# Performance work log

Hardware: AMD Instinct MI355X
Metric: run time of the kernel (lower is better)

## Reference

```python
import jax, jax.numpy as jnp
import numpy as np

EPS = 1e-12  # F.normalize default eps


def _wn_weight(v, g):
    # torch weight_norm(dim=0) on Conv1d weight [out, in, 1]: w = g * v / ||v||_rows
    norm = jnp.sqrt(jnp.sum(v * v, axis=1, keepdims=True))
    return v * (g[:, None] / norm)


def _l2norm(x):
    n = jnp.sqrt(jnp.sum(x * x, axis=-1, keepdims=True))
    return x / jnp.maximum(n, EPS)


def setup_inputs() -> dict:
    key = jax.random.key(0)
    ks = jax.random.split(key, 4)
    B, D, T = 16, 1024, 4096
    CD, CS = 8, 1024
    return {
        "z": jax.random.normal(ks[0], (B, D, T), dtype=jnp.float32),
        "in_proj_v": jax.random.normal(ks[1], (CD, D), dtype=jnp.float32) * 0.02,
        "in_proj_g": jnp.ones((CD,), dtype=jnp.float32),
        "in_proj_b": jnp.zeros((CD,), dtype=jnp.float32),
        "out_proj_v": jax.random.normal(ks[2], (D, CD), dtype=jnp.float32) * 0.02,
        "out_proj_g": jnp.ones((D,), dtype=jnp.float32),
        "out_proj_b": jnp.zeros((D,), dtype=jnp.float32),
        "codebook": jax.random.normal(ks[3], (CS, CD), dtype=jnp.float32),
    }


def reference(z, in_proj_v, in_proj_g, in_proj_b, out_proj_v, out_proj_g, out_proj_b, codebook):
    B, D, T = z.shape
    CD = codebook.shape[1]

    # in_proj: 1x1 weight-normed conv == per-timestep linear
    w_in = _wn_weight(in_proj_v, in_proj_g)            # [CD, D]
    z_e = jnp.einsum('od,bdt->bot', w_in, z) + in_proj_b[None, :, None]  # [B, CD, T]

    # decode_latents: cosine-distance nearest neighbor in normalized space
    enc = jnp.transpose(z_e, (0, 2, 1)).reshape(B * T, CD)  # (b t) d
    enc_n = _l2norm(enc)
    cb_n = _l2norm(codebook)
    # dist = |e|^2 - 2 e.c + |c|^2 over normalized vectors
    dist = (jnp.sum(enc_n * enc_n, axis=1, keepdims=True)
            - 2.0 * enc_n @ cb_n.T
            + jnp.sum(cb_n * cb_n, axis=1)[None, :])       # [B*T, CS]
    indices = jnp.argmax(-dist, axis=1).reshape(B, T)      # [B, T]
    z_q = jnp.transpose(codebook[indices], (0, 2, 1))      # [B, CD, T] (un-normalized codebook gather)

    # losses (reduce over dims [1,2] -> per-batch)
    sg = jax.lax.stop_gradient
    commitment_loss = jnp.mean((z_e - sg(z_q)) ** 2, axis=(1, 2))
    codebook_loss = jnp.mean((z_q - sg(z_e)) ** 2, axis=(1, 2))

    # straight-through
    z_q_st = z_e + sg(z_q - z_e)

    w_out = _wn_weight(out_proj_v, out_proj_g)          # [D, CD]
    out = jnp.einsum('dc,bct->bdt', w_out, z_q_st) + out_proj_b[None, :, None]
    return out, commitment_loss, codebook_loss, indices, z_e
```

## Files before the change

kernel.cpp:

```cpp
#include <hip/hip_runtime.h>
#include <math.h>

#define BB 16
#define DD 1024
#define TT 4096
#define CD 8
#define CS 1024

#define OFF_LOSS_C 67108864
#define OFF_LOSS_B 67108880
#define OFF_IDX    67108896
#define OFF_ZE     67174432

#define WS_WIN  0
#define WS_WOUT 8192
#define WS_CBN  16384
#define WS_CS   24576

#define TILE_T 64

typedef float vfloat4 __attribute__((ext_vector_type(4)));

__global__ __launch_bounds__(256) void prep_kernel(
    const float* __restrict__ in_v,
    const float* __restrict__ in_g,
    const float* __restrict__ out_v,
    const float* __restrict__ out_g,
    const float* __restrict__ cb,
    float* __restrict__ ws)
{
    int bid = blockIdx.x, tid = threadIdx.x;
    if (bid < 8) {
        __shared__ float red[256];
        __shared__ float ssc;
        int o = bid;
        float p = 0.f;
        for (int k = tid; k < DD; k += 256) { float v = in_v[o*DD + k]; p += v*v; }
        red[tid] = p; __syncthreads();
        for (int s = 128; s > 0; s >>= 1) { if (tid < s) red[tid] += red[tid+s]; __syncthreads(); }
        if (tid == 0) ssc = in_g[o] / sqrtf(red[0]);
        __syncthreads();
        float scale = ssc;
        for (int d = tid; d < DD; d += 256)
            ws[WS_WIN + d*CD + o] = in_v[o*DD + d] * scale;
    } else if (bid < 12) {
        int d = (bid - 8) * 256 + tid;
        float v[CD]; float ssq = 0.f;
        #pragma unroll
        for (int c = 0; c < CD; ++c) { v[c] = out_v[d*CD + c]; ssq += v[c]*v[c]; }
        float s = out_g[d] / sqrtf(ssq);
        #pragma unroll
        for (int c = 0; c < CD; ++c) ws[WS_WOUT + d*CD + c] = v[c]*s;
    } else {
        int c = (bid - 12) * 256 + tid;
        double* csh = (double*)(ws + WS_CS);
        float v[CD]; float ssq = 0.f;
        #pragma unroll
        for (int j = 0; j < CD; ++j) { v[j] = cb[c*CD + j]; ssq += v[j]*v[j]; }
        float n = fmaxf(sqrtf(ssq), 1e-12f);
        double sq = 0.0;
        #pragma unroll
        for (int j = 0; j < CD; ++j) {
            float e = v[j] / n;
            ws[WS_CBN + c*CD + j] = e;
            sq = fma((double)e, (double)e, sq);
        }
        csh[c] = 0.5 * sq;
    }
}

__global__ __launch_bounds__(256, 4) void fused_kernel(
    const float* __restrict__ z,
    const float* __restrict__ in_b,
    const float* __restrict__ cb,
    const float* __restrict__ out_b,
    const float* __restrict__ ws,
    float* __restrict__ outb)
{
    __shared__ float  zpart[4][CD][TILE_T];
    __shared__ float  ze_s[CD][TILE_T];
    __shared__ float  nrm_s[TILE_T];
    __shared__ double best_s[4][TILE_T];
    __shared__ int    bidx_s[4][TILE_T];
    __shared__ __align__(16) float zq_s[CD][TILE_T];

    int tid  = threadIdx.x;
    int b    = blockIdx.y;
    int t0   = blockIdx.x * TILE_T;
    int tl   = tid & 63;
    int wv   = __builtin_amdgcn_readfirstlane(tid >> 6);

    {
        const float* zp = z + ((size_t)(b*DD + wv*256)) * TT + t0 + tl;
        const float* w  = ws + WS_WIN + wv*256*CD;
        float acc[CD];
        #pragma unroll
        for (int o = 0; o < CD; ++o) acc[o] = 0.f;
        #pragma unroll 16
        for (int j = 0; j < 256; ++j) {
            float zv = zp[(size_t)j * TT];
            #pragma unroll
            for (int o = 0; o < CD; ++o) acc[o] = fmaf(w[j*CD + o], zv, acc[o]);
        }
        #pragma unroll
        for (int o = 0; o < CD; ++o) zpart[wv][o][tl] = acc[o];
    }
    __syncthreads();

    #pragma unroll
    for (int p = tid; p < CD*TILE_T; p += 256) {
        int o = p >> 6, t = p & 63;
        float v = in_b[o] + ((zpart[0][o][t] + zpart[1][o][t]) +
                             (zpart[2][o][t] + zpart[3][o][t]));
        ze_s[o][t] = v;
        outb[OFF_ZE + ((size_t)(b*CD + o)) * TT + t0 + t] = v;
    }
    __syncthreads();
    if (tid < TILE_T) {
        float ssq = 0.f;
        #pragma unroll
        for (int o = 0; o < CD; ++o) { float vv = ze_s[o][tid]; ssq = fmaf(vv, vv, ssq); }
        nrm_s[tid] = fmaxf(sqrtf(ssq), 1e-12f);
    }
    __syncthreads();

    {
        int t = tl;
        float nr = nrm_s[t];
        double en[CD];
        #pragma unroll
        for (int o = 0; o < CD; ++o) en[o] = (double)(ze_s[o][t] / nr);
        const float*  cbn = ws + WS_CBN;
        const double* csh = (const double*)(ws + WS_CS);
        int c0 = wv * 256;
        double best = -1.0e300; int bi = c0;
        for (int c = c0; c < c0 + 256; ++c) {
            float cr[CD];
            *(float4*)&cr[0] = *(const float4*)(cbn + c*CD);
            *(float4*)&cr[4] = *(const float4*)(cbn + c*CD + 4);
            double dot = 0.0;
            #pragma unroll
            for (int o = 0; o < CD; ++o) dot = fma((double)cr[o], en[o], dot);
            double score = dot - csh[c];
            if (score > best) { best = score; bi = c; }
        }
        best_s[wv][t] = best; bidx_s[wv][t] = bi;
    }
    __syncthreads();

    if (tid < TILE_T) {
        int t = tid;
        double best = best_s[0][t]; int bi = bidx_s[0][t];
        #pragma unroll
        for (int k = 1; k < 4; ++k) {
            if (best_s[k][t] > best) { best = best_s[k][t]; bi = bidx_s[k][t]; }
        }
        outb[OFF_IDX + b*TT + t0 + t] = (float)bi;

        float q[CD];
        *(float4*)&q[0] = *(const float4*)(cb + bi*CD);
        *(float4*)&q[4] = *(const float4*)(cb + bi*CD + 4);
        #pragma unroll
        for (int o = 0; o < CD; ++o) zq_s[o][t] = q[o];

        float l = 0.f;
        #pragma unroll
        for (int o = 0; o < CD; ++o) { float d = ze_s[o][t] - q[o]; l = fmaf(d, d, l); }
        #pragma unroll
        for (int off = 32; off > 0; off >>= 1) l += __shfl_down(l, off, 64);
        if (tid == 0) {
            float s = l * (1.0f / (CD * TT));
            atomicAdd(outb + OFF_LOSS_C + b, s);
            atomicAdd(outb + OFF_LOSS_B + b, s);
        }
    }
    __syncthreads();

    {
        int tq = tid & 15;
        int dg = tid >> 4;
        float4 qv[CD];
        #pragma unroll
        for (int o = 0; o < CD; ++o) qv[o] = *(const float4*)&zq_s[o][tq*4];

        size_t obase = (size_t)b * DD * TT + t0 + tq*4;
        const float4* wv4 = (const float4*)(ws + WS_WOUT);
        #pragma unroll 4
        for (int i = 0; i < 64; ++i) {
            int d = i*16 + dg;
            float wr[CD];
            *(float4*)&wr[0] = wv4[2*d];
            *(float4*)&wr[4] = wv4[2*d + 1];
            float bbv = out_b[d];
            vfloat4 r = { bbv, bbv, bbv, bbv };
            #pragma unroll
            for (int o = 0; o < CD; ++o) {
                float wo = wr[o];
                r.x = fmaf(wo, qv[o].x, r.x);
                r.y = fmaf(wo, qv[o].y, r.y);
                r.z = fmaf(wo, qv[o].z, r.z);
                r.w = fmaf(wo, qv[o].w, r.w);
            }
            __builtin_nontemporal_store(r, (vfloat4*)(outb + obase + (size_t)d * TT));
        }
    }
}

extern "C" void kernel_launch(void* const* d_in, const int* in_sizes, int n_in,
                              void* d_out, int out_size, void* d_ws, size_t ws_size,
                              hipStream_t stream) {
    const float* z     = (const float*)d_in[0];
    const float* in_v  = (const float*)d_in[1];
    const float* in_g  = (const float*)d_in[2];
    const float* in_b  = (const float*)d_in[3];
    const float* out_v = (const float*)d_in[4];
    const float* out_g = (const float*)d_in[5];
    const float* out_b = (const float*)d_in[6];
    const float* cb    = (const float*)d_in[7];
    float* ws  = (float*)d_ws;
    float* out = (float*)d_out;

    (void)hipMemsetAsync(out + OFF_LOSS_C, 0, 32 * sizeof(float), stream);

    prep_kernel<<<16, 256, 0, stream>>>(in_v, in_g, out_v, out_g, cb, ws);
    fused_kernel<<<dim3(TT/TILE_T, BB), 256, 0, stream>>>(z, in_b, cb, out_b, ws, out);
}
```

Before: 546.9 us.

## Split fused VQ kernel into in-proj partial, VQ, and out-proj kernels

Splits the single fused kernel into three: an input-projection kernel that writes per-D-chunk partial sums, a VQ kernel that reduces those partials and runs the argmax search, and an out-projection kernel that gathers codewords from the stored indices. The partials are parked in the (not yet written) output buffer region. The in-projection now loads float4 of z per thread, and the out-projection uses its own grid over time and D chunks. The aim is to decouple the bandwidth-bound z read and output write from the compute-heavy search so each stage can use a better tiling and occupancy. In exchange it adds kernel launches and an extra global round trip for the partials and indices. The in-projection grid is also small (256 blocks with long per-thread loops), which may limit memory parallelism.

```diff
diff --git a/kernel.cpp b/kernel.cpp
--- a/kernel.cpp
+++ b/kernel.cpp
@@ -11,13 +11,12 @@
 #define OFF_LOSS_B 67108880
 #define OFF_IDX    67108896
 #define OFF_ZE     67174432
+#define OFF_PART   0
 
 #define WS_WIN  0
 #define WS_WOUT 8192
 #define WS_CBN  16384
 #define WS_CS   24576
-
-#define TILE_T 64
 
 typedef float vfloat4 __attribute__((ext_vector_type(4)));
 
@@ -69,54 +68,75 @@
     }
 }
 
-__global__ __launch_bounds__(256, 4) void fused_kernel(
+__global__ __launch_bounds__(256) void zpart_kernel(
     const float* __restrict__ z,
+    const float* __restrict__ ws,
+    float* __restrict__ outb)
+{
+    int tid  = threadIdx.x;
+    int lane = tid & 63;
+    int wv   = __builtin_amdgcn_readfirstlane(tid >> 6);
+    int tg = blockIdx.x, dc = blockIdx.y, b = blockIdx.z;
+    int tc = tg * 4 + wv;
+    int t0 = tc * 256;
+
+    const float* zp = z + ((size_t)(b*DD + dc*256)) * TT + t0 + lane*4;
+    const float* w  = ws + WS_WIN + dc*256*CD;
+
+    float4 acc[CD];
+    #pragma unroll
+    for (int o = 0; o < CD; ++o) acc[o] = make_float4(0.f, 0.f, 0.f, 0.f);
+
+    #pragma unroll 8
+    for (int j = 0; j < 256; ++j) {
+        float4 zv = *(const float4*)(zp + (size_t)j * TT);
+        #pragma unroll
+        for (int o = 0; o < CD; ++o) {
+            float wo = w[j*CD + o];
+            acc[o].x = fmaf(wo, zv.x, acc[o].x);
+            acc[o].y = fmaf(wo, zv.y, acc[o].y);
+            acc[o].z = fmaf(wo, zv.z, acc[o].z);
+            acc[o].w = fmaf(wo, zv.w, acc[o].w);
+        }
+    }
+
+    size_t pbase = ((size_t)(b*4 + dc)) * CD * TT + t0 + lane*4;
+    #pragma unroll
+    for (int o = 0; o < CD; ++o)
+        *(float4*)(outb + OFF_PART + pbase + (size_t)o * TT) = acc[o];
+}
+
+__global__ __launch_bounds__(256) void vq_kernel(
     const float* __restrict__ in_b,
     const float* __restrict__ cb,
-    const float* __restrict__ out_b,
     const float* __restrict__ ws,
     float* __restrict__ outb)
 {
-    __shared__ float  zpart[4][CD][TILE_T];
-    __shared__ float  ze_s[CD][TILE_T];
-    __shared__ float  nrm_s[TILE_T];
-    __shared__ double best_s[4][TILE_T];
-    __shared__ int    bidx_s[4][TILE_T];
-    __shared__ __align__(16) float zq_s[CD][TILE_T];
-
-    int tid  = threadIdx.x;
-    int b    = blockIdx.y;
-    int t0   = blockIdx.x * TILE_T;
-    int tl   = tid & 63;
-    int wv   = __builtin_amdgcn_readfirstlane(tid >> 6);
-
-    {
-        const float* zp = z + ((size_t)(b*DD + wv*256)) * TT + t0 + tl;
-        const float* w  = ws + WS_WIN + wv*256*CD;
-        float acc[CD];
-        #pragma unroll
-        for (int o = 0; o < CD; ++o) acc[o] = 0.f;
-        #pragma unroll 16
-        for (int j = 0; j < 256; ++j) {
-            float zv = zp[(size_t)j * TT];
-            #pragma unroll
-            for (int o = 0; o < CD; ++o) acc[o] = fmaf(w[j*CD + o], zv, acc[o]);
-        }
-        #pragma unroll
-        for (int o = 0; o < CD; ++o) zpart[wv][o][tl] = acc[o];
-    }
-    __syncthreads();
-
-    #pragma unroll
-    for (int p = tid; p < CD*TILE_T; p += 256) {
+    __shared__ float  ze_s[CD][64];
+    __shared__ float  nrm_s[64];
+    __shared__ double best_s[4][64];
+    __shared__ int    bidx_s[4][64];
+
+    int tid = threadIdx.x;
+    int b   = blockIdx.y;
+    int t0  = blockIdx.x * 64;
+    int tl  = tid & 63;
+    int wv  = __builtin_amdgcn_readfirstlane(tid >> 6);
+
+    #pragma unroll
+    for (int p = tid; p < CD*64; p += 256) {
         int o = p >> 6, t = p & 63;
-        float v = in_b[o] + ((zpart[0][o][t] + zpart[1][o][t]) +
-                             (zpart[2][o][t] + zpart[3][o][t]));
+        size_t pb = (size_t)(b*4) * CD * TT + (size_t)o * TT + t0 + t;
+        float v0 = outb[OFF_PART + pb];
+        float v1 = outb[OFF_PART + pb + (size_t)CD*TT];
+        float v2 = outb[OFF_PART + pb + (size_t)2*CD*TT];
+        float v3 = outb[OFF_PART + pb + (size_t)3*CD*TT];
+        float v = in_b[o] + ((v0 + v1) + (v2 + v3));
         ze_s[o][t] = v;
         outb[OFF_ZE + ((size_t)(b*CD + o)) * TT + t0 + t] = v;
     }
     __syncthreads();
-    if (tid < TILE_T) {
+    if (tid < 64) {
         float ssq = 0.f;
         #pragma unroll
         for (int o = 0; o < CD; ++o) { float vv = ze_s[o][tid]; ssq = fmaf(vv, vv, ssq); }
@@ -148,7 +168,7 @@
     }
     __syncthreads();
 
-    if (tid < TILE_T) {
+    if (tid < 64) {
         int t = tid;
         double best = best_s[0][t]; int bi = bidx_s[0][t];
         #pragma unroll
@@ -160,9 +180,6 @@
         float q[CD];
         *(float4*)&q[0] = *(const float4*)(cb + bi*CD);
         *(float4*)&q[4] = *(const float4*)(cb + bi*CD + 4);
-        #pragma unroll
-        for (int o = 0; o < CD; ++o) zq_s[o][t] = q[o];
-
         float l = 0.f;
         #pragma unroll
         for (int o = 0; o < CD; ++o) { float d = ze_s[o][t] - q[o]; l = fmaf(d, d, l); }
@@ -174,35 +191,54 @@
             atomicAdd(outb + OFF_LOSS_B + b, s);
         }
     }
-    __syncthreads();
+}
+
+__global__ __launch_bounds__(256) void out_proj_kernel(
+    const float* __restrict__ cb,
+    const float* __restrict__ out_b,
+    const float* __restrict__ ws,
+    float* __restrict__ outb)
+{
+    __shared__ __align__(16) float zq_s[CD][256];
+
+    int tid = threadIdx.x;
+    int tc = blockIdx.x, dch = blockIdx.y, b = blockIdx.z;
+    int t0 = tc * 256;
 
     {
-        int tq = tid & 15;
-        int dg = tid >> 4;
-        float4 qv[CD];
-        #pragma unroll
-        for (int o = 0; o < CD; ++o) qv[o] = *(const float4*)&zq_s[o][tq*4];
-
-        size_t obase = (size_t)b * DD * TT + t0 + tq*4;
-        const float4* wv4 = (const float4*)(ws + WS_WOUT);
-        #pragma unroll 4
-        for (int i = 0; i < 64; ++i) {
-            int d = i*16 + dg;
-            float wr[CD];
-            *(float4*)&wr[0] = wv4[2*d];
-            *(float4*)&wr[4] = wv4[2*d + 1];
-            float bbv = out_b[d];
-            vfloat4 r = { bbv, bbv, bbv, bbv };
-            #pragma unroll
-            for (int o = 0; o < CD; ++o) {
-                float wo = wr[o];
-                r.x = fmaf(wo, qv[o].x, r.x);
-                r.y = fmaf(wo, qv[o].y, r.y);
-                r.z = fmaf(wo, qv[o].z, r.z);
-                r.w = fmaf(wo, qv[o].w, r.w);
-            }
-            __builtin_nontemporal_store(r, (vfloat4*)(outb + obase + (size_t)d * TT));
-        }
+        int bi = (int)outb[OFF_IDX + b*TT + t0 + tid];
+        const float4* cr = (const float4*)(cb + bi*CD);
+        float4 q0 = cr[0], q1 = cr[1];
+        zq_s[0][tid] = q0.x; zq_s[1][tid] = q0.y; zq_s[2][tid] = q0.z; zq_s[3][tid] = q0.w;
+        zq_s[4][tid] = q1.x; zq_s[5][tid] = q1.y; zq_s[6][tid] = q1.z; zq_s[7][tid] = q1.w;
+    }
+    __syncthreads();
+
+    int lane = tid & 63;
+    int wv   = tid >> 6;
+    float4 qv[CD];
+    #pragma unroll
+    for (int o = 0; o < CD; ++o) qv[o] = *(const float4*)&zq_s[o][lane*4];
+
+    int dbase = dch*256 + wv*64;
+    size_t obase = ((size_t)(b*DD + dbase)) * TT + t0 + lane*4;
+    const float* wp = ws + WS_WOUT + dbase*CD;
+    #pragma unroll 4
+    for (int i = 0; i < 64; ++i) {
+        float wr[CD];
+        *(float4*)&wr[0] = *(const float4*)(wp + i*CD);
+        *(float4*)&wr[4] = *(const float4*)(wp + i*CD + 4);
+        float bbv = out_b[dbase + i];
+        vfloat4 r = { bbv, bbv, bbv, bbv };
+        #pragma unroll
+        for (int o = 0; o < CD; ++o) {
+            float wo = wr[o];
+            r.x = fmaf(wo, qv[o].x, r.x);
+            r.y = fmaf(wo, qv[o].y, r.y);
+            r.z = fmaf(wo, qv[o].z, r.z);
+            r.w = fmaf(wo, qv[o].w, r.w);
+        }
+        __builtin_nontemporal_store(r, (vfloat4*)(outb + obase + (size_t)i * TT));
     }
 }
 
@@ -223,5 +259,7 @@
     (void)hipMemsetAsync(out + OFF_LOSS_C, 0, 32 * sizeof(float), stream);
 
     prep_kernel<<<16, 256, 0, stream>>>(in_v, in_g, out_v, out_g, cb, ws);
-    fused_kernel<<<dim3(TT/TILE_T, BB), 256, 0, stream>>>(z, in_b, cb, out_b, ws, out);
-}
+    zpart_kernel<<<dim3(4, 4, BB), 256, 0, stream>>>(z, ws, out);
+    vq_kernel<<<dim3(TT/64, BB), 256, 0, stream>>>(in_b, cb, ws, out);
+    out_proj_kernel<<<dim3(16, 4, BB), 256, 0, stream>>>(cb, out_b, ws, out);
+}
```

After: 536.3 us. About the same (-1.9%).
